# Performance work log

Measured on AMD Instinct MI355X. Metric: run time of the kernel, lower is better.

## Reference

```python
import jax, jax.numpy as jnp
import numpy as np

# Hyper-params from init_kwargs
H, DM, DA, DP, M, T = 8, 512, 256, 128, 32, 4096
DK, DAh, DPh = DM // H, DA // H, DP // H   # 64, 32, 16
B, K_STEPS = 8, 2048
S = T + K_STEPS          # length of x = memory + x_pre
EPS = 1e-12

def _l2n(x):
    # F.normalize(p=2, dim=-1)
    return x / jnp.maximum(jnp.linalg.norm(x, axis=-1, keepdims=True), EPS)

def setup_inputs() -> dict:
    key = jax.random.key(0)
    ks = jax.random.split(key, 28)
    n = lambda i, s, sc=0.05: jax.random.normal(ks[i], s, jnp.float32) * sc
    return {
        "memory": jax.random.normal(ks[0], (B, S - 1, DM), jnp.float32),
        "x_pre":  jax.random.normal(ks[1], (B, 1, DM), jnp.float32),
        "aux":    jax.random.normal(ks[2], (B, S, DA), jnp.float32),
        "pos":    jax.random.normal(ks[3], (B, S, DP), jnp.float32),
        "Wq": n(4, (H, DK, DM)), "bq": n(5, (H, DK)),
        "Wk": n(6, (H, DK, DM)), "bk": n(7, (H, DK)),
        "Wv": n(8, (H, DK, DM)), "bv": n(9, (H, DK)),
        "Wqa": n(10, (H, DAh, DA)), "bqa": n(11, (H, DAh)),
        "Wka": n(12, (H, DAh, DA)), "bka": n(13, (H, DAh)),
        "Wqp": n(14, (H, DPh, DP)), "bqp": n(15, (H, DPh)),
        "Wkp": n(16, (H, DPh, DP)), "bkp": n(17, (H, DPh)),
        "W_ih": n(18, (3 * DK, DM)), "W_hh": n(19, (3 * DK, DK)),
        "b_ih": n(20, (3 * DK,)), "b_hh": n(21, (3 * DK,)),
        "WO": n(22, (DM, DM)), "bO": n(23, (DM,)),
        "w": n(24, (1, 1), 1.0), "w_a": n(25, (1, 1), 1.0), "w_p": n(26, (1, 1), 1.0),
        "G": (jax.random.uniform(ks[27], (DK, DK)) < 0.5).astype(jnp.int32),
        "k": K_STEPS,
    }

def _forward(memory, x_pre, aux, pos, Wq, bq, Wk, bk, Wv, bv, Wqa, bqa, Wka, bka,
             Wqp, bqp, Wkp, bkp, W_ih, W_hh, b_ih, b_hh, WO, bO, w, w_a, w_p, G, k):
    b = memory.shape[0]
    x = jnp.concatenate([memory, x_pre], axis=1)           # [B, S, DM]
    s = x.shape[1]
    Wn = k + T - M + 1                                     # attention window length
    g = G.astype(x.dtype)
    mask_h = jnp.tile(g, (1, H))[None]                     # [1, DK, DM] per-head SparseLinear mask

    # per-head Q/K node projections (SparseLinear), L2-normalized
    Q = _l2n(jnp.einsum('bsd,hkd->bhsk', x, Wq * mask_h) + bq[None, :, None, :])
    K = _l2n(jnp.einsum('bsd,hkd->bhsk', x, Wk * mask_h) + bk[None, :, None, :])

    # tn_transform_pre: for each position p, mean over the M-step window of Qv[m].K[p+m]
    Qv = Q[:, :, -M:, :]                                   # [B,H,M,DK]
    D = jnp.einsum('bhmd,bhsd->bhms', Qv, K)               # [B,H,M,S]
    p_idx = jnp.arange(Wn)[None, :] + jnp.arange(M)[:, None]   # [M,Wn]
    band = D[:, :, jnp.arange(M)[:, None], p_idx]          # [B,H,M,Wn] band-diagonal gather
    tn = band.mean(axis=2)                                 # [B,H,Wn]

    # aux / pos similarities: only the last query row survives the slice in the source
    QA = _l2n(jnp.einsum('bsa,hca->bhsc', aux, Wqa) + bqa[None, :, None, :])
    KA = _l2n(jnp.einsum('bsa,hca->bhsc', aux, Wka) + bka[None, :, None, :])
    dot2 = jnp.einsum('bhc,bhsc->bhs', QA[:, :, -1, :], KA[:, :, aux.shape[1] - Wn:, :])
    QP = _l2n(jnp.einsum('bsp,hcp->bhsc', pos, Wqp) + bqp[None, :, None, :])
    KP = _l2n(jnp.einsum('bsp,hcp->bhsc', pos, Wkp) + bkp[None, :, None, :])
    dot3 = jnp.einsum('bhc,bhsc->bhs', QP[:, :, -1, :], KP[:, :, pos.shape[1] - Wn:, :])

    attn = jax.nn.softmax(w[0, 0] * tn + w_a[0, 0] * dot2 + w_p[0, 0] * dot3, axis=-1)  # [B,H,Wn]

    # value projection over the history window, weighted by attn[..., :-1]
    xv = x[:, s - Wn:s - 1, :]                             # [B, Wn-1, DM]
    V = jnp.einsum('bsd,hkd->bhsk', xv, Wv * mask_h) + bv[None, :, None, :]
    hist = jnp.einsum('bhw,bhwd->bhd', attn[:, :, :-1], V) # [B,H,DK]

    # sequential GRU over the recent M-1 steps (shared across heads)
    recent = jnp.swapaxes(x[:, -M:-1, :], 0, 1)            # [M-1, B, DM]
    def cell(hprev, xt):
        gi = xt @ W_ih.T + b_ih
        gh = hprev @ W_hh.T + b_hh
        ir, iz, inn = jnp.split(gi, 3, axis=-1)
        hr, hz, hn = jnp.split(gh, 3, axis=-1)
        r = jax.nn.sigmoid(ir + hr)
        z = jax.nn.sigmoid(iz + hz)
        nst = jnp.tanh(inn + r * hn)
        return (1.0 - z) * nst + z * hprev, None
    res, _ = jax.lax.scan(cell, jnp.zeros((b, DK), x.dtype), recent)  # [B, DK]

    # concat per-head deltas (deta[:, :, 1:] just drops the initial zeros column)
    deta = (hist + attn[:, :, -1:] * res[:, None, :]).reshape(b, H * DK)   # [B, DM]
    mask_o = jnp.tile(g, (H, H))                           # [DM, DM] for W_O
    out = x_pre + (deta @ (WO * mask_o).T + bO)[:, None, :]
    return out

def reference(memory, x_pre, aux, pos, Wq, bq, Wk, bk, Wv, bv, Wqa, bqa, Wka, bka,
              Wqp, bqp, Wkp, bkp, W_ih, W_hh, b_ih, b_hh, WO, bO, w, w_a, w_p, G, k):
    return _forward(memory, x_pre, aux, pos, Wq, bq, Wk, bk, Wv, bv, Wqa, bqa, Wka,
                    bka, Wqp, bqp, Wkp, bkp, W_ih, W_hh, b_ih, b_hh, WO, bO,
                    w, w_a, w_p, G, k)
```

## Files before the change

kernel.cpp:

```cpp
#include <hip/hip_runtime.h>
#include <math.h>

#define BB   8
#define S    6144
#define SM1  6143
#define DM   512
#define H    8
#define DK   64
#define M    32
#define WN   6113
#define DA   256
#define DAh  32
#define DP   128
#define DPh  16
#define EPSN 1e-12f

#define WS_WKT    0
#define WS_WKAT   262144
#define WS_WKPT   327680
#define WS_QHAT   344064
#define WS_QAHAT  475136
#define WS_QPHAT  477184
#define WS_LOGITS 478208
#define WS_XBAR   869440
#define WS_ALAST  902208
#define WS_RES    902272
#define WS_GI     902784
#define WS_WQM    950400
#define WS_XBF    1212544
#define N_LOGITS  391232
#define N_XBAR    32768

typedef __attribute__((ext_vector_type(8))) short short8;
typedef __attribute__((ext_vector_type(4))) float f32x4;

__device__ inline unsigned short f2bf(float f) {
    union { float f; unsigned u; } v; v.f = f;
    unsigned r = v.u + 0x7fffu + ((v.u >> 16) & 1u);
    return (unsigned short)(r >> 16);
}
__device__ inline float bf2f(unsigned short u) {
    union { unsigned u; float f; } v; v.u = ((unsigned)u) << 16; return v.f;
}

union S8U { short8 v; unsigned short e[8]; };

__global__ void prep_weights(const float* __restrict__ Wk, const float* __restrict__ Wka,
                             const float* __restrict__ Wkp, const float* __restrict__ Wq,
                             const int* __restrict__ G,
                             unsigned short* __restrict__ wkb,
                             unsigned short* __restrict__ wkab,
                             unsigned short* __restrict__ wkpb,
                             float* __restrict__ wqm)
{
    int idx = blockIdx.x * 256 + threadIdx.x;
    if (idx < H*DM*DK) {
        int k = idx & 63; int d = (idx >> 6) & 511; int h = idx >> 15;
        float v = Wk[(size_t)(h*DK + k)*DM + d] * (float)G[k*DK + (d & 63)];
        wkb[(size_t)h*DM*DK + (((d >> 3)*DK + k) << 3) + (d & 7)] = f2bf(v);
    }
    int i2 = idx - H*DM*DK;
    if (i2 >= 0 && i2 < H*DA*DAh) {
        int h = i2 >> 13; int r = i2 & 8191;
        int j = r & 7; int f = r >> 3;
        int c = f & 31; int a = (f >> 5)*8 + j;
        wkab[i2] = f2bf(Wka[(size_t)(h*DAh + c)*DA + a]);
    }
    int i3 = idx - H*DM*DK - H*DA*DAh;
    if (i3 >= 0 && i3 < H*DP*DPh) {
        int h = i3 >> 11; int r = i3 & 2047;
        int j = r & 7; int f = r >> 3;
        int c = f & 15; int p = (f >> 4)*8 + j;
        wkpb[i3] = f2bf(Wkp[(size_t)(h*DPh + c)*DP + p]);
    }
    int i4 = idx - H*DM*DK - H*DA*DAh - H*DP*DPh;
    if (i4 >= 0 && i4 < H*DK*DM) {
        int d = i4 & 511; int k = (i4 >> 9) & 63;
        wqm[i4] = Wq[i4] * (float)G[k*DK + (d & 63)];
    }
}

__global__ __launch_bounds__(256) void xcast_k(
    const float* __restrict__ memory, const float* __restrict__ x_pre,
    unsigned short* __restrict__ xbf)
{
    size_t e = ((size_t)blockIdx.x*256 + threadIdx.x)*8;
    int b = (int)(e / ((size_t)S*DM));
    size_t r = e - (size_t)b*S*DM;
    int t = (int)(r >> 9);
    int d = (int)(r & 511);
    const float* src = (t < SM1) ? memory + ((size_t)b*SM1 + t)*DM + d
                                 : x_pre + (size_t)b*DM + d;
    float4 v0 = *(const float4*)src, v1 = *(const float4*)(src + 4);
    S8U t8;
    t8.e[0]=f2bf(v0.x); t8.e[1]=f2bf(v0.y); t8.e[2]=f2bf(v0.z); t8.e[3]=f2bf(v0.w);
    t8.e[4]=f2bf(v1.x); t8.e[5]=f2bf(v1.y); t8.e[6]=f2bf(v1.z); t8.e[7]=f2bf(v1.w);
    *(short8*)(xbf + e) = t8.v;
}

__global__ __launch_bounds__(256) void qhat_k2(
    const float* __restrict__ memory, const float* __restrict__ x_pre,
    const float* __restrict__ wqm, const float* __restrict__ bq,
    float* __restrict__ qhat)
{
    int bx = blockIdx.x;
    int mp = bx & 15;
    int h  = (bx >> 4) & 7;
    int b  = bx >> 7;
    int tid = threadIdx.x;
    int k = tid & 63, dq = tid >> 6;

    int m0 = mp*2;
    int t0 = S - M + m0, t1 = t0 + 1;
    const float* x0 = ((t0 < SM1) ? memory + ((size_t)b*SM1 + t0)*DM
                                  : x_pre + (size_t)b*DM) + dq*128;
    const float* x1 = ((t1 < SM1) ? memory + ((size_t)b*SM1 + t1)*DM
                                  : x_pre + (size_t)b*DM) + dq*128;
    const float* wr = wqm + (size_t)(h*DK + k)*DM + dq*128;

    float s0 = 0.f, s1 = 0.f;
    #pragma unroll 8
    for (int d = 0; d < 128; d += 4) {
        float4 w4 = *(const float4*)(wr + d);
        float4 a4 = *(const float4*)(x0 + d);
        float4 b4 = *(const float4*)(x1 + d);
        s0 += w4.x*a4.x + w4.y*a4.y + w4.z*a4.z + w4.w*a4.w;
        s1 += w4.x*b4.x + w4.y*b4.y + w4.z*b4.z + w4.w*b4.w;
    }

    __shared__ float part[2][4][64];
    part[0][dq][k] = s0;
    part[1][dq][k] = s1;
    __syncthreads();

    if (tid < 128) {
        int mi = tid >> 6;
        int kk = tid & 63;
        float q = part[mi][0][kk] + part[mi][1][kk] + part[mi][2][kk] + part[mi][3][kk]
                + bq[h*DK + kk];
        float ss = q*q;
        #pragma unroll
        for (int d2 = 1; d2 <= 32; d2 <<= 1) ss += __shfl_xor(ss, d2);
        qhat[((size_t)(b*H + h)*M + (m0 + mi))*DK + kk] = q / fmaxf(sqrtf(ss), EPSN);
    }
}

__global__ __launch_bounds__(256) void qaqp_k(
    const float* __restrict__ aux, const float* __restrict__ pos,
    const float* __restrict__ Wqa, const float* __restrict__ bqa,
    const float* __restrict__ Wqp, const float* __restrict__ bqp,
    float* __restrict__ qahat, float* __restrict__ qphat)
{
    int bh = blockIdx.x; int b = bh >> 3, h = bh & 7;
    int tid = threadIdx.x;
    __shared__ float pa[32][8];
    __shared__ float pp[16][16];

    {
        int c = tid & 31, ch = tid >> 5;
        const float* ar = aux + ((size_t)b*S + (S-1))*DA + ch*32;
        const float* wv = Wqa + (size_t)(h*DAh + c)*DA + ch*32;
        float s = 0.f;
        #pragma unroll
        for (int a = 0; a < 32; a += 4) {
            float4 a4 = *(const float4*)(ar + a);
            float4 w4 = *(const float4*)(wv + a);
            s += a4.x*w4.x + a4.y*w4.y + a4.z*w4.z + a4.w*w4.w;
        }
        pa[c][ch] = s;
    }
    {
        int c = tid & 15, ch = tid >> 4;
        const float* pr = pos + ((size_t)b*S + (S-1))*DP + ch*8;
        const float* wv = Wqp + (size_t)(h*DPh + c)*DP + ch*8;
        float4 a4 = *(const float4*)(pr);
        float4 w4 = *(const float4*)(wv);
        float4 a5 = *(const float4*)(pr + 4);
        float4 w5 = *(const float4*)(wv + 4);
        pp[c][ch] = a4.x*w4.x + a4.y*w4.y + a4.z*w4.z + a4.w*w4.w
                  + a5.x*w5.x + a5.y*w5.y + a5.z*w5.z + a5.w*w5.w;
    }
    __syncthreads();

    if (tid < 32) {
        float q = bqa[h*DAh + tid];
        #pragma unroll
        for (int ch = 0; ch < 8; ++ch) q += pa[tid][ch];
        float ss = q*q;
        #pragma unroll
        for (int d2 = 1; d2 <= 16; d2 <<= 1) ss += __shfl_xor(ss, d2);
        qahat[(size_t)bh*DAh + tid] = q / fmaxf(sqrtf(ss), EPSN);
    } else if (tid >= 64 && tid < 80) {
        int c = tid - 64;
        float q = bqp[h*DPh + c];
        #pragma unroll
        for (int ch = 0; ch < 16; ++ch) q += pp[c][ch];
        float ss = q*q;
        #pragma unroll
        for (int d2 = 1; d2 <= 8; d2 <<= 1) ss += __shfl_xor(ss, d2);
        qphat[(size_t)bh*DPh + c] = q / fmaxf(sqrtf(ss), EPSN);
    }
}

__global__ __launch_bounds__(256, 4) void kproj_mfma3(
    const unsigned short* __restrict__ xbf, const unsigned short* __restrict__ wkb,
    const float* __restrict__ bk, const float* __restrict__ qhat,
    const float* __restrict__ wscal, float* __restrict__ logits)
{
    int bx = blockIdx.x;
    int tile = bx % 96, h = (bx / 96) & 7, b = bx / (96*8);
    int t0 = tile * 64;
    int tid = threadIdx.x;
    int wave = tid >> 6, lane = tid & 63;
    int quad = lane >> 4, l16 = lane & 15;

    __shared__ unsigned short Qs[M][72];
    __shared__ unsigned short Kb[64][72];
    __shared__ float tnloc[95];

    {
        const float* qsrc = qhat + (size_t)(b*H + h)*M*DK;
        int i = tid * 8;
        float4 a0 = *(const float4*)(qsrc + i);
        float4 a1 = *(const float4*)(qsrc + i + 4);
        S8U t8;
        t8.e[0]=f2bf(a0.x); t8.e[1]=f2bf(a0.y); t8.e[2]=f2bf(a0.z); t8.e[3]=f2bf(a0.w);
        t8.e[4]=f2bf(a1.x); t8.e[5]=f2bf(a1.y); t8.e[6]=f2bf(a1.z); t8.e[7]=f2bf(a1.w);
        *(short8*)&Qs[i >> 6][i & 63] = t8.v;
    }
    if (tid < 95) tnloc[tid] = 0.f;

    f32x4 acc[4];
    #pragma unroll
    for (int nt = 0; nt < 4; ++nt) acc[nt] = (f32x4){0.f,0.f,0.f,0.f};

    const unsigned short* xrow = xbf + ((size_t)b*S + t0 + wave*16 + l16)*DM;
    const unsigned short* wh = wkb + (size_t)h*DM*DK;

    #pragma unroll
    for (int ch = 0; ch < 4; ++ch) {
        #pragma unroll
        for (int ks = 0; ks < 4; ++ks) {
            short8 a = *(const short8*)(xrow + ch*128 + ks*32 + quad*8);
            #pragma unroll
            for (int nt = 0; nt < 4; ++nt) {
                short8 bf = *(const short8*)(wh + (((ch*16 + ks*4 + quad)*DK) + nt*16 + l16)*8);
                acc[nt] = __builtin_amdgcn_mfma_f32_16x16x32_bf16(a, bf, acc[nt], 0, 0, 0);
            }
        }
    }

    {
        float vv[4][4];
        float ss[4] = {0.f, 0.f, 0.f, 0.f};
        #pragma unroll
        for (int nt = 0; nt < 4; ++nt) {
            float bkv = bk[h*DK + nt*16 + l16];
            #pragma unroll
            for (int reg = 0; reg < 4; ++reg) {
                float v = acc[nt][reg] + bkv;
                vv[nt][reg] = v;
                ss[reg] += v*v;
            }
        }
        #pragma unroll
        for (int d2 = 1; d2 <= 8; d2 <<= 1)
            #pragma unroll
            for (int reg = 0; reg < 4; ++reg) ss[reg] += __shfl_xor(ss[reg], d2);
        #pragma unroll
        for (int reg = 0; reg < 4; ++reg) {
            float inv = 1.f / fmaxf(sqrtf(ss[reg]), EPSN);
            #pragma unroll
            for (int nt = 0; nt < 4; ++nt)
                Kb[wave*16 + quad*4 + reg][nt*16 + l16] = f2bf(vv[nt][reg] * inv);
        }
    }
    __syncthreads();

    {
        int mtile = wave & 1;
        int thalf = (wave >> 1) * 32;
        f32x4 acc2[2];
        acc2[0] = (f32x4){0.f,0.f,0.f,0.f};
        acc2[1] = (f32x4){0.f,0.f,0.f,0.f};
        #pragma unroll
        for (int ks = 0; ks < 2; ++ks) {
            short8 a = *(const short8*)&Qs[mtile*16 + l16][ks*32 + quad*8];
            #pragma unroll
            for (int nt = 0; nt < 2; ++nt) {
                short8 kf = *(const short8*)&Kb[thalf + nt*16 + l16][ks*32 + quad*8];
                acc2[nt] = __builtin_amdgcn_mfma_f32_16x16x32_bf16(a, kf, acc2[nt], 0, 0, 0);
            }
        }
        int m0 = mtile*16 + quad*4;
        #pragma unroll
        for (int nt = 0; nt < 2; ++nt) {
            int tl = thalf + nt*16 + l16;
            #pragma unroll
            for (int reg = 0; reg < 4; ++reg) {
                int mm = m0 + reg;
                int j = t0 + tl - mm;
                if (j >= 0 && j < WN)
                    atomicAdd(&tnloc[tl - mm + 31], acc2[nt][reg]);
            }
        }
    }
    __syncthreads();
    if (tid < 95) {
        int j = t0 + tid - 31;
        if (j >= 0 && j < WN)
            atomicAdd(&logits[(size_t)(b*H + h)*WN + j], wscal[0]*(1.f/32.f)*tnloc[tid]);
    }
}

__global__ __launch_bounds__(256, 2) void ka_proj_mfma(
    const float* __restrict__ aux, const unsigned short* __restrict__ wkab,
    const float* __restrict__ bka, const float* __restrict__ qahat,
    const float* __restrict__ wa, float* __restrict__ logits)
{
    int tile = blockIdx.x % 96;
    int b    = blockIdx.x / 96;
    int j0   = tile * 64;
    int tid  = threadIdx.x;
    int wave = tid >> 6, lane = tid & 63;
    int quad = lane >> 4, l16 = lane & 15;

    __shared__ unsigned short Xa[32*520];

    {
        int r = tid >> 2, seg = tid & 3;
        int j = j0 + r; if (j > WN-1) j = WN-1;
        const float* ar = aux + ((size_t)b*S + (31 + j))*DA + seg*64;
        int tt = r >> 4, lo = r & 15;
        #pragma unroll
        for (int g = 0; g < 8; ++g) {
            float4 v0 = *(const float4*)(ar + g*8);
            float4 v1 = *(const float4*)(ar + g*8 + 4);
            int d0 = seg*64 + g*8;
            int ks = d0 >> 5, qd = (d0 >> 3) & 3;
            S8U t8;
            t8.e[0]=f2bf(v0.x); t8.e[1]=f2bf(v0.y); t8.e[2]=f2bf(v0.z); t8.e[3]=f2bf(v0.w);
            t8.e[4]=f2bf(v1.x); t8.e[5]=f2bf(v1.y); t8.e[6]=f2bf(v1.z); t8.e[7]=f2bf(v1.w);
            *(short8*)&Xa[(tt*8 + ks)*520 + (qd*16 + lo)*8] = t8.v;
        }
    }
    __syncthreads();

    float wav = wa[0];
    for (int h = 0; h < H; ++h) {
        const unsigned short* wsrc = wkab + (size_t)h*DA*DAh;
        f32x4 acc[2];
        acc[0] = (f32x4){0.f,0.f,0.f,0.f};
        acc[1] = (f32x4){0.f,0.f,0.f,0.f};
        #pragma unroll
        for (int ks = 0; ks < 8; ++ks) {
            short8 a = *(const short8*)&Xa[(wave*8 + ks)*520 + lane*8];
            #pragma unroll
            for (int nt = 0; nt < 2; ++nt) {
                short8 bf = *(const short8*)(wsrc + (size_t)(((ks*4 + quad)*32) + nt*16 + l16)*8);
                acc[nt] = __builtin_amdgcn_mfma_f32_16x16x32_bf16(a, bf, acc[nt], 0, 0, 0);
            }
        }
        float bk0 = bka[h*DAh + l16], bk1 = bka[h*DAh + 16 + l16];
        float q0 = qahat[(size_t)(b*H + h)*DAh + l16];
        float q1 = qahat[(size_t)(b*H + h)*DAh + 16 + l16];
        #pragma unroll
        for (int reg = 0; reg < 4; ++reg) {
            float v0 = acc[0][reg] + bk0;
            float v1 = acc[1][reg] + bk1;
            float ss = v0*v0 + v1*v1;
            float dp = v0*q0 + v1*q1;
            #pragma unroll
            for (int d2 = 1; d2 <= 8; d2 <<= 1) {
                ss += __shfl_xor(ss, d2);
                dp += __shfl_xor(dp, d2);
            }
            if (l16 == 0) {
                int j = j0 + wave*16 + quad*4 + reg;
                if (j < WN)
                    logits[(size_t)(b*H + h)*WN + j] += wav * dp / fmaxf(sqrtf(ss), EPSN);
            }
        }
    }
}

__global__ __launch_bounds__(256, 2) void kp_proj_mfma(
    const float* __restrict__ pos, const unsigned short* __restrict__ wkpb,
    const float* __restrict__ bkp, const float* __restrict__ qphat,
    const float* __restrict__ wp, float* __restrict__ logits)
{
    int tile = blockIdx.x % 96;
    int b    = blockIdx.x / 96;
    int j0   = tile * 64;
    int tid  = threadIdx.x;
    int wave = tid >> 6, lane = tid & 63;
    int quad = lane >> 4, l16 = lane & 15;

    __shared__ unsigned short Xp[16*520];

    {
        int r = tid >> 2, seg = tid & 3;
        int j = j0 + r; if (j > WN-1) j = WN-1;
        const float* pr = pos + ((size_t)b*S + (31 + j))*DP + seg*32;
        int tt = r >> 4, lo = r & 15;
        #pragma unroll
        for (int g = 0; g < 4; ++g) {
            float4 v0 = *(const float4*)(pr + g*8);
            float4 v1 = *(const float4*)(pr + g*8 + 4);
            int d0 = seg*32 + g*8;
            int ks = d0 >> 5, qd = (d0 >> 3) & 3;
            S8U t8;
            t8.e[0]=f2bf(v0.x); t8.e[1]=f2bf(v0.y); t8.e[2]=f2bf(v0.z); t8.e[3]=f2bf(v0.w);
            t8.e[4]=f2bf(v1.x); t8.e[5]=f2bf(v1.y); t8.e[6]=f2bf(v1.z); t8.e[7]=f2bf(v1.w);
            *(short8*)&Xp[(tt*4 + ks)*520 + (qd*16 + lo)*8] = t8.v;
        }
    }
    __syncthreads();

    float wpv = wp[0];
    for (int h = 0; h < H; ++h) {
        const unsigned short* wsrc = wkpb + (size_t)h*DP*DPh;
        f32x4 acc = (f32x4){0.f,0.f,0.f,0.f};
        #pragma unroll
        for (int ks = 0; ks < 4; ++ks) {
            short8 a = *(const short8*)&Xp[(wave*4 + ks)*520 + lane*8];
            short8 bf = *(const short8*)(wsrc + (size_t)(((ks*4 + quad)*16) + l16)*8);
            acc = __builtin_amdgcn_mfma_f32_16x16x32_bf16(a, bf, acc, 0, 0, 0);
        }
        float bk0 = bkp[h*DPh + l16];
        float q0 = qphat[(size_t)(b*H + h)*DPh + l16];
        #pragma unroll
        for (int reg = 0; reg < 4; ++reg) {
            float v = acc[reg] + bk0;
            float ss = v*v;
            float dp = v*q0;
            #pragma unroll
            for (int d2 = 1; d2 <= 8; d2 <<= 1) {
                ss += __shfl_xor(ss, d2);
                dp += __shfl_xor(dp, d2);
            }
            if (l16 == 0) {
                int j = j0 + wave*16 + quad*4 + reg;
                if (j < WN)
                    logits[(size_t)(b*H + h)*WN + j] += wpv * dp / fmaxf(sqrtf(ss), EPSN);
            }
        }
    }
}

__global__ __launch_bounds__(256, 2) void kproj_band_mfma2(
    const float* __restrict__ memory, const float* __restrict__ x_pre,
    const unsigned short* __restrict__ wkb, const float* __restrict__ bk,
    const float* __restrict__ qhat, const float* __restrict__ wscal,
    float* __restrict__ logits)
{
    int bx = blockIdx.x;
    int hp = bx & 3, b = (bx >> 2) & 7, tile = bx >> 5;
    int t0 = tile * 128;
    int tid = threadIdx.x;
    int wave = tid >> 6, lane = tid & 63;
    int quad = lane >> 4, l16 = lane & 15;

    __shared__ unsigned short Xf[32*520];
    __shared__ unsigned short Wf[16*520];
    __shared__ unsigned short Kb[128][72];
    __shared__ unsigned short Qs[M][72];
    __shared__ float tnloc[159];

    if (tid < 159) tnloc[tid] = 0.f;
    {
        int h = hp*2;
        const float* qsrc = qhat + (size_t)(b*H + h)*M*DK;
        int i = tid * 8;
        float4 a0 = *(const float4*)(qsrc + i);
        float4 a1 = *(const float4*)(qsrc + i + 4);
        S8U t8;
        t8.e[0]=f2bf(a0.x); t8.e[1]=f2bf(a0.y); t8.e[2]=f2bf(a0.z); t8.e[3]=f2bf(a0.w);
        t8.e[4]=f2bf(a1.x); t8.e[5]=f2bf(a1.y); t8.e[6]=f2bf(a1.z); t8.e[7]=f2bf(a1.w);
        *(short8*)&Qs[i >> 6][i & 63] = t8.v;
    }

    f32x4 acc[2][2][4];
    #pragma unroll
    for (int hi = 0; hi < 2; ++hi)
        #pragma unroll
        for (int mt = 0; mt < 2; ++mt)
            #pragma unroll
            for (int nt = 0; nt < 4; ++nt) acc[hi][mt][nt] = (f32x4){0.f,0.f,0.f,0.f};

    for (int ch = 0; ch < 4; ++ch) {
        __syncthreads();
        {
            int r = tid >> 1, half = tid & 1;
            int t = t0 + r;
            const float* xr = ((t < SM1) ? (memory + ((size_t)b*SM1 + t)*DM)
                                         : (x_pre + (size_t)b*DM)) + ch*128 + half*64;
            int tt = r >> 4, lo = r & 15;
            #pragma unroll
            for (int g = 0; g < 8; ++g) {
                float4 v0 = *(const float4*)(xr + g*8);
                float4 v1 = *(const float4*)(xr + g*8 + 4);
                int d0 = half*64 + g*8;
                int ks = d0 >> 5, qd = (d0 >> 3) & 3;
                S8U t8;
                t8.e[0]=f2bf(v0.x); t8.e[1]=f2bf(v0.y); t8.e[2]=f2bf(v0.z); t8.e[3]=f2bf(v0.w);
                t8.e[4]=f2bf(v1.x); t8.e[5]=f2bf(v1.y); t8.e[6]=f2bf(v1.z); t8.e[7]=f2bf(v1.w);
                *(short8*)&Xf[(tt*4 + ks)*520 + (qd*16 + lo)*8] = t8.v;
            }
        }
        {
            const unsigned short* src = wkb + (size_t)(hp*2)*DM*DK + (size_t)ch*8192;
            #pragma unroll
            for (int i = 0; i < 4; ++i) {
                int f = tid + 256*i;
                *(short8*)&Wf[(f >> 6)*520 + (f & 63)*8] = *(const short8*)(src + f*8);
            }
        }
        __syncthreads();
        #pragma unroll
        for (int ks = 0; ks < 4; ++ks) {
            short8 a0 = *(const short8*)&Xf[((wave*2 + 0)*4 + ks)*520 + lane*8];
            short8 a1 = *(const short8*)&Xf[((wave*2 + 1)*4 + ks)*520 + lane*8];
            #pragma unroll
            for (int nt = 0; nt < 4; ++nt) {
                short8 bf = *(const short8*)&Wf[(ks*4 + quad)*520 + (nt*16 + l16)*8];
                acc[0][0][nt] = __builtin_amdgcn_mfma_f32_16x16x32_bf16(a0, bf, acc[0][0][nt], 0, 0, 0);
                acc[0][1][nt] = __builtin_amdgcn_mfma_f32_16x16x32_bf16(a1, bf, acc[0][1][nt], 0, 0, 0);
            }
        }
        __syncthreads();
        {
            const unsigned short* src = wkb + (size_t)(hp*2 + 1)*DM*DK + (size_t)ch*8192;
            #pragma unroll
            for (int i = 0; i < 4; ++i) {
                int f = tid + 256*i;
                *(short8*)&Wf[(f >> 6)*520 + (f & 63)*8] = *(const short8*)(src + f*8);
            }
        }
        __syncthreads();
        #pragma unroll
        for (int ks = 0; ks < 4; ++ks) {
            short8 a0 = *(const short8*)&Xf[((wave*2 + 0)*4 + ks)*520 + lane*8];
            short8 a1 = *(const short8*)&Xf[((wave*2 + 1)*4 + ks)*520 + lane*8];
            #pragma unroll
            for (int nt = 0; nt < 4; ++nt) {
                short8 bf = *(const short8*)&Wf[(ks*4 + quad)*520 + (nt*16 + l16)*8];
                acc[1][0][nt] = __builtin_amdgcn_mfma_f32_16x16x32_bf16(a0, bf, acc[1][0][nt], 0, 0, 0);
                acc[1][1][nt] = __builtin_amdgcn_mfma_f32_16x16x32_bf16(a1, bf, acc[1][1][nt], 0, 0, 0);
            }
        }
    }

    float wom = wscal[0] * (1.f/32.f);

    for (int hi = 0; hi < 2; ++hi) {
        int h = hp*2 + hi;
        __syncthreads();
        {
            float ss[2][4];
            float vv[2][4][4];
            #pragma unroll
            for (int mt = 0; mt < 2; ++mt)
                #pragma unroll
                for (int reg = 0; reg < 4; ++reg) ss[mt][reg] = 0.f;
            #pragma unroll
            for (int nt = 0; nt < 4; ++nt) {
                float bkv = bk[h*DK + nt*16 + l16];
                #pragma unroll
                for (int mt = 0; mt < 2; ++mt)
                    #pragma unroll
                    for (int reg = 0; reg < 4; ++reg) {
                        float v = acc[hi][mt][nt][reg] + bkv;
                        vv[mt][nt][reg] = v;
                        ss[mt][reg] += v*v;
                    }
            }
            #pragma unroll
            for (int d2 = 1; d2 <= 8; d2 <<= 1)
                #pragma unroll
                for (int mt = 0; mt < 2; ++mt)
                    #pragma unroll
                    for (int reg = 0; reg < 4; ++reg)
                        ss[mt][reg] += __shfl_xor(ss[mt][reg], d2);
            #pragma unroll
            for (int mt = 0; mt < 2; ++mt) {
                float inv[4];
                #pragma unroll
                for (int reg = 0; reg < 4; ++reg)
                    inv[reg] = 1.f / fmaxf(sqrtf(ss[mt][reg]), EPSN);
                #pragma unroll
                for (int nt = 0; nt < 4; ++nt)
                    #pragma unroll
                    for (int reg = 0; reg < 4; ++reg)
                        Kb[wave*32 + mt*16 + quad*4 + reg][nt*16 + l16] =
                            f2bf(vv[mt][nt][reg] * inv[reg]);
            }
        }
        __syncthreads();
        {
            f32x4 acc2[2][2];
            #pragma unroll
            for (int mt = 0; mt < 2; ++mt)
                #pragma unroll
                for (int nt = 0; nt < 2; ++nt) acc2[mt][nt] = (f32x4){0.f,0.f,0.f,0.f};
            #pragma unroll
            for (int ks = 0; ks < 2; ++ks) {
                short8 qa0 = *(const short8*)&Qs[l16     ][ks*32 + quad*8];
                short8 qa1 = *(const short8*)&Qs[16 + l16][ks*32 + quad*8];
                #pragma unroll
                for (int nt = 0; nt < 2; ++nt) {
                    short8 kf = *(const short8*)&Kb[wave*32 + nt*16 + l16][ks*32 + quad*8];
                    acc2[0][nt] = __builtin_amdgcn_mfma_f32_16x16x32_bf16(qa0, kf, acc2[0][nt], 0, 0, 0);
                    acc2[1][nt] = __builtin_amdgcn_mfma_f32_16x16x32_bf16(qa1, kf, acc2[1][nt], 0, 0, 0);
                }
            }
            #pragma unroll
            for (int mt = 0; mt < 2; ++mt)
                #pragma unroll
                for (int nt = 0; nt < 2; ++nt) {
                    int tcol = wave*32 + nt*16 + l16;
                    #pragma unroll
                    for (int reg = 0; reg < 4; ++reg) {
                        int m = mt*16 + quad*4 + reg;
                        int j = t0 + tcol - m;
                        if (j >= 0 && j < WN)
                            atomicAdd(&tnloc[tcol - m + 31], acc2[mt][nt][reg]);
                    }
                }
        }
        __syncthreads();
        if (tid < 159) {
            int j = t0 + tid - 31;
            if (j >= 0 && j < WN)
                atomicAdd(&logits[(size_t)(b*H + h)*WN + j], wom * tnloc[tid]);
            tnloc[tid] = 0.f;
        }
        if (hi == 0) {
            const float* qsrc = qhat + (size_t)(b*H + h + 1)*M*DK;
            int i = tid * 8;
            float4 a0 = *(const float4*)(qsrc + i);
            float4 a1 = *(const float4*)(qsrc + i + 4);
            S8U t8;
            t8.e[0]=f2bf(a0.x); t8.e[1]=f2bf(a0.y); t8.e[2]=f2bf(a0.z); t8.e[3]=f2bf(a0.w);
            t8.e[4]=f2bf(a1.x); t8.e[5]=f2bf(a1.y); t8.e[6]=f2bf(a1.z); t8.e[7]=f2bf(a1.w);
            *(short8*)&Qs[i >> 6][i & 63] = t8.v;
        }
    }
}

__global__ __launch_bounds__(256) void softmax_k(float* __restrict__ logits,
                                                 float* __restrict__ alast)
{
    int bh = blockIdx.x;
    float* L = logits + (size_t)bh*WN;
    __shared__ float red[256];
    int tid = threadIdx.x;
    float mx = -1e30f;
    for (int j = tid; j < WN; j += 256) mx = fmaxf(mx, L[j]);
    red[tid] = mx; __syncthreads();
    for (int s2 = 128; s2 > 0; s2 >>= 1) {
        if (tid < s2) red[tid] = fmaxf(red[tid], red[tid+s2]);
        __syncthreads();
    }
    mx = red[0]; __syncthreads();
    float sm = 0.f;
    for (int j = tid; j < WN; j += 256) sm += expf(L[j] - mx);
    red[tid] = sm; __syncthreads();
    for (int s2 = 128; s2 > 0; s2 >>= 1) {
        if (tid < s2) red[tid] += red[tid+s2];
        __syncthreads();
    }
    float inv = 1.f / red[0];
    for (int j = tid; j < WN; j += 256) {
        float a = expf(L[j] - mx) * inv;
        L[j] = a;
        if (j == WN-1) alast[bh] = a;
    }
}

#define JC 191
__global__ __launch_bounds__(256) void xbar_bf_k(
    const unsigned short* __restrict__ xbf, const float* __restrict__ attn,
    float* __restrict__ xbar)
{
    int chunk = blockIdx.x & 31;
    int b = blockIdx.x >> 5;
    int j0 = chunk * JC;
    __shared__ float al[H][JC];
    int tid = threadIdx.x;
    for (int i = tid; i < H*JC; i += 256) {
        int hh = i / JC, jj = i - hh*JC;
        al[hh][jj] = attn[(size_t)(b*H + hh)*WN + j0 + jj];
    }
    __syncthreads();
    int d0 = tid * 2;
    const unsigned* p = (const unsigned*)(xbf + ((size_t)b*S + 31 + j0)*DM + d0);
    float acc[H][2];
    #pragma unroll
    for (int hh = 0; hh < H; ++hh) { acc[hh][0] = 0.f; acc[hh][1] = 0.f; }
    for (int jj = 0; jj < JC; ++jj) {
        unsigned u = p[(size_t)jj*(DM/2)];
        float x0 = bf2f((unsigned short)(u & 0xffff));
        float x1 = bf2f((unsigned short)(u >> 16));
        #pragma unroll
        for (int hh = 0; hh < H; ++hh) {
            float a = al[hh][jj];
            acc[hh][0] += a * x0;
            acc[hh][1] += a * x1;
        }
    }
    #pragma unroll
    for (int hh = 0; hh < H; ++hh) {
        atomicAdd(&xbar[(size_t)(b*H+hh)*DM + d0],     acc[hh][0]);
        atomicAdd(&xbar[(size_t)(b*H+hh)*DM + d0 + 1], acc[hh][1]);
    }
}

__global__ __launch_bounds__(256) void xbar_k(
    const float* __restrict__ memory, const float* __restrict__ attn,
    float* __restrict__ xbar)
{
    int chunk = blockIdx.x & 31;
    int b = blockIdx.x >> 5;
    int j0 = chunk * JC;
    __shared__ float al[H][JC];
    int tid = threadIdx.x;
    for (int i = tid; i < H*JC; i += 256) {
        int hh = i / JC, jj = i - hh*JC;
        al[hh][jj] = attn[(size_t)(b*H + hh)*WN + j0 + jj];
    }
    __syncthreads();
    int d0 = tid * 2;
    float acc[H][2];
    #pragma unroll
    for (int hh = 0; hh < H; ++hh) { acc[hh][0] = 0.f; acc[hh][1] = 0.f; }
    for (int jj = 0; jj < JC; ++jj) {
        int t = 31 + j0 + jj;
        const float2 xv = *(const float2*)(memory + ((size_t)b*SM1 + t)*DM + d0);
        #pragma unroll
        for (int hh = 0; hh < H; ++hh) {
            float a = al[hh][jj];
            acc[hh][0] += a * xv.x;
            acc[hh][1] += a * xv.y;
        }
    }
    #pragma unroll
    for (int hh = 0; hh < H; ++hh) {
        atomicAdd(&xbar[(size_t)(b*H+hh)*DM + d0],     acc[hh][0]);
        atomicAdd(&xbar[(size_t)(b*H+hh)*DM + d0 + 1], acc[hh][1]);
    }
}

__global__ __launch_bounds__(192) void gi_k(
    const float* __restrict__ memory, const float* __restrict__ W_ih,
    const float* __restrict__ b_ih, float* __restrict__ gi_all)
{
    int t = blockIdx.x >> 3;
    int b = blockIdx.x & 7;
    int c = threadIdx.x;
    const float* xr = memory + ((size_t)b*SM1 + (S - M) + t)*DM;
    const float* wr = W_ih + (size_t)c*DM;
    float s = b_ih[c];
    for (int d = 0; d < DM; d += 4) {
        float4 x4 = *(const float4*)(xr + d);
        float4 w4 = *(const float4*)(wr + d);
        s += x4.x*w4.x + x4.y*w4.y + x4.z*w4.z + x4.w*w4.w;
    }
    gi_all[((size_t)t*BB + b)*192 + c] = s;
}

__global__ __launch_bounds__(512) void gru_scan(
    const float* __restrict__ gi_all, const float* __restrict__ W_hh,
    const float* __restrict__ b_hh, float* __restrict__ res)
{
    int b = threadIdx.x >> 6;
    int l = threadIdx.x & 63;

    float w0[64], w1[64], w2[64];
    {
        const float* r0p = W_hh + (size_t)l*DK;
        const float* r1p = W_hh + (size_t)(64 + l)*DK;
        const float* r2p = W_hh + (size_t)(128 + l)*DK;
        #pragma unroll
        for (int i = 0; i < 16; ++i) {
            float4 a = *(const float4*)(r0p + i*4);
            w0[i*4]=a.x; w0[i*4+1]=a.y; w0[i*4+2]=a.z; w0[i*4+3]=a.w;
            float4 c = *(const float4*)(r1p + i*4);
            w1[i*4]=c.x; w1[i*4+1]=c.y; w1[i*4+2]=c.z; w1[i*4+3]=c.w;
            float4 e = *(const float4*)(r2p + i*4);
            w2[i*4]=e.x; w2[i*4+1]=e.y; w2[i*4+2]=e.z; w2[i*4+3]=e.w;
        }
    }
    float bh0 = b_hh[l], bh1 = b_hh[64 + l], bh2 = b_hh[128 + l];

    float h = 0.f;
    const float* g0 = gi_all + (size_t)b*192;
    float gr = g0[l], gz = g0[64 + l], gn = g0[128 + l];

    #pragma unroll 1
    for (int t = 0; t < 31; ++t) {
        float a0 = bh0, a1 = bh1, a2 = bh2;
        #pragma unroll
        for (int k = 0; k < 64; ++k) {
            float hk = __int_as_float(__builtin_amdgcn_readlane(__float_as_int(h), k));
            a0 += hk * w0[k];
            a1 += hk * w1[k];
            a2 += hk * w2[k];
        }
        float ngr = 0.f, ngz = 0.f, ngn = 0.f;
        if (t < 30) {
            const float* g2 = gi_all + ((size_t)(t+1)*BB + b)*192;
            ngr = g2[l]; ngz = g2[64 + l]; ngn = g2[128 + l];
        }
        float r = 1.f / (1.f + expf(-(gr + a0)));
        float z = 1.f / (1.f + expf(-(gz + a1)));
        float n = tanhf(gn + r * a2);
        h = (1.f - z)*n + z*h;
        gr = ngr; gz = ngz; gn = ngn;
    }
    res[b*DK + l] = h;
}

__global__ __launch_bounds__(512) void final_k(
    const float* __restrict__ x_pre, const float* __restrict__ xbar,
    const float* __restrict__ Wv, const float* __restrict__ bv,
    const float* __restrict__ WO, const float* __restrict__ bO,
    const float* __restrict__ alast, const float* __restrict__ res,
    const int* __restrict__ G, float* __restrict__ out)
{
    int b = blockIdx.x;
    int tid = threadIdx.x;
    __shared__ float gl[64*64];
    __shared__ float deta[512];
    for (int i = tid; i < 4096; i += 512) gl[i] = (float)G[(i & 63)*64 + (i >> 6)];
    __syncthreads();
    int h = tid >> 6, dk = tid & 63;
    float ala = alast[b*H + h];
    const float* xb  = xbar + (size_t)(b*H + h)*DM;
    const float* wvr = Wv + (size_t)tid*DM;
    const float* gcol = gl + dk;
    float s = 0.f;
    for (int e = 0; e < DM; e += 4) {
        float4 wv4 = *(const float4*)(wvr + e);
        float4 xb4 = *(const float4*)(xb + e);
        int eb = e & 63;
        s += wv4.x*gcol[eb*64]     *xb4.x + wv4.y*gcol[(eb+1)*64]*xb4.y
           + wv4.z*gcol[(eb+2)*64]*xb4.z + wv4.w*gcol[(eb+3)*64]*xb4.w;
    }
    float hist = s + bv[tid]*(1.f - ala);
    deta[tid] = hist + ala * res[b*DK + dk];
    __syncthreads();
    int dpos = tid;
    const float* wor = WO + (size_t)dpos*DM;
    const float* gcol2 = gl + (dpos & 63);
    float o = 0.f;
    for (int jj = 0; jj < DM; jj += 4) {
        float4 wo4 = *(const float4*)(wor + jj);
        int jb = jj & 63;
        o += wo4.x*gcol2[jb*64]     *deta[jj]   + wo4.y*gcol2[(jb+1)*64]*deta[jj+1]
           + wo4.z*gcol2[(jb+2)*64]*deta[jj+2] + wo4.w*gcol2[(jb+3)*64]*deta[jj+3];
    }
    out[(size_t)b*DM + dpos] = x_pre[(size_t)b*DM + dpos] + o + bO[dpos];
}

extern "C" void kernel_launch(void* const* d_in, const int* in_sizes, int n_in,
                              void* d_out, int out_size, void* d_ws, size_t ws_size,
                              hipStream_t stream)
{
    const float* memory = (const float*)d_in[0];
    const float* x_pre  = (const float*)d_in[1];
    const float* aux    = (const float*)d_in[2];
    const float* pos    = (const float*)d_in[3];
    const float* Wq  = (const float*)d_in[4];
    const float* bq  = (const float*)d_in[5];
    const float* Wk  = (const float*)d_in[6];
    const float* bk  = (const float*)d_in[7];
    const float* Wv  = (const float*)d_in[8];
    const float* bv  = (const float*)d_in[9];
    const float* Wqa = (const float*)d_in[10];
    const float* bqa = (const float*)d_in[11];
    const float* Wka = (const float*)d_in[12];
    const float* bka = (const float*)d_in[13];
    const float* Wqp = (const float*)d_in[14];
    const float* bqp = (const float*)d_in[15];
    const float* Wkp = (const float*)d_in[16];
    const float* bkp = (const float*)d_in[17];
    const float* W_ih = (const float*)d_in[18];
    const float* W_hh = (const float*)d_in[19];
    const float* b_ih = (const float*)d_in[20];
    const float* b_hh = (const float*)d_in[21];
    const float* WO  = (const float*)d_in[22];
    const float* bO  = (const float*)d_in[23];
    const float* w   = (const float*)d_in[24];
    const float* w_a = (const float*)d_in[25];
    const float* w_p = (const float*)d_in[26];
    const int*   G   = (const int*)d_in[27];
    (void)in_sizes; (void)n_in; (void)out_size;

    float* ws = (float*)d_ws;
    unsigned short* wkb  = (unsigned short*)(ws + WS_WKT);
    unsigned short* wkab = (unsigned short*)(ws + WS_WKAT);
    unsigned short* wkpb = (unsigned short*)(ws + WS_WKPT);
    float* qhat   = ws + WS_QHAT;
    float* qahat  = ws + WS_QAHAT;
    float* qphat  = ws + WS_QPHAT;
    float* logits = ws + WS_LOGITS;
    float* xbar   = ws + WS_XBAR;
    float* alast  = ws + WS_ALAST;
    float* resb   = ws + WS_RES;
    float* gi_all = ws + WS_GI;
    float* wqm    = ws + WS_WQM;
    unsigned short* xbf = (unsigned short*)(ws + WS_XBF);
    float* outp   = (float*)d_out;

    const size_t need = ((size_t)WS_XBF + 12582912) * 4;
    const bool big = (ws_size >= need);

    hipMemsetAsync(logits, 0, (size_t)(N_LOGITS + N_XBAR)*sizeof(float), stream);

    prep_weights<<<(H*DM*DK + H*DA*DAh + H*DP*DPh + H*DK*DM + 255)/256, 256, 0, stream>>>(
        Wk, Wka, Wkp, Wq, G, wkb, wkab, wkpb, wqm);

    if (big)
        xcast_k<<<12288, 256, 0, stream>>>(memory, x_pre, xbf);

    gi_k<<<31*BB, 192, 0, stream>>>(memory, W_ih, b_ih, gi_all);
    gru_scan<<<1, 512, 0, stream>>>(gi_all, W_hh, b_hh, resb);

    qhat_k2<<<BB*H*16, 256, 0, stream>>>(memory, x_pre, wqm, bq, qhat);
    qaqp_k<<<BB*H, 256, 0, stream>>>(aux, pos, Wqa, bqa, Wqp, bqp, qahat, qphat);

    if (big)
        kproj_mfma3<<<96*8*BB, 256, 0, stream>>>(xbf, wkb, bk, qhat, w, logits);
    else
        kproj_band_mfma2<<<48*BB*4, 256, 0, stream>>>(memory, x_pre, wkb, bk, qhat,
                                                      w, logits);

    ka_proj_mfma<<<BB*96, 256, 0, stream>>>(aux, wkab, bka, qahat, w_a, logits);
    kp_proj_mfma<<<BB*96, 256, 0, stream>>>(pos, wkpb, bkp, qphat, w_p, logits);

    softmax_k<<<BB*H, 256, 0, stream>>>(logits, alast);

    if (big)
        xbar_bf_k<<<BB*32, 256, 0, stream>>>(xbf, logits, xbar);
    else
        xbar_k<<<BB*32, 256, 0, stream>>>(memory, logits, xbar);

    final_k<<<BB, 512, 0, stream>>>(x_pre, xbar, Wv, bv, WO, bO, alast, resb, G, outp);
}
```

Before: 614.0 us.

## Retile K projection so one block covers all heads with shared A tiles

The bf16 copy of x is rewritten into a k-slot-major layout of 8-element groups, produced through a shared-memory transpose. The K projection kernel now runs 512-thread blocks where each wave handles one head for a 64-row tile. Activation tiles are loaded once into double-buffered LDS and reused across all eight heads, instead of each head's block re-reading x. Q is pre-packed into bf16 MFMA fragment order by a new qhat kernel, and the Kb tile uses XOR swizzling against bank conflicts. This adds per-step barriers, a larger register footprint (16 accumulators per wave), and a layout change that the xbar kernel must also follow.

```diff
diff --git a/kernel.cpp b/kernel.cpp
--- a/kernel.cpp
+++ b/kernel.cpp
@@ -80,22 +80,44 @@
     }
 }
 
-__global__ __launch_bounds__(256) void xcast_k(
+__global__ __launch_bounds__(256) void xcast2_k(
     const float* __restrict__ memory, const float* __restrict__ x_pre,
-    unsigned short* __restrict__ xbf)
-{
-    size_t e = ((size_t)blockIdx.x*256 + threadIdx.x)*8;
-    int b = (int)(e / ((size_t)S*DM));
-    size_t r = e - (size_t)b*S*DM;
-    int t = (int)(r >> 9);
-    int d = (int)(r & 511);
-    const float* src = (t < SM1) ? memory + ((size_t)b*SM1 + t)*DM + d
-                                 : x_pre + (size_t)b*DM + d;
-    float4 v0 = *(const float4*)src, v1 = *(const float4*)(src + 4);
-    S8U t8;
-    t8.e[0]=f2bf(v0.x); t8.e[1]=f2bf(v0.y); t8.e[2]=f2bf(v0.z); t8.e[3]=f2bf(v0.w);
-    t8.e[4]=f2bf(v1.x); t8.e[5]=f2bf(v1.y); t8.e[6]=f2bf(v1.z); t8.e[7]=f2bf(v1.w);
-    *(short8*)(xbf + e) = t8.v;
+    unsigned short* __restrict__ xbf2)
+{
+    int tile = blockIdx.x % 96;
+    int b    = blockIdx.x / 96;
+    int t0 = tile * 64;
+    int tid = threadIdx.x;
+    __shared__ __align__(16) unsigned short T[64][72];
+
+    int tr = tid >> 2, seg = tid & 3;
+    int t  = t0 + tr;
+    const float* src = (t < SM1) ? memory + ((size_t)b*SM1 + t)*DM
+                                 : x_pre + (size_t)b*DM;
+
+    for (int dch = 0; dch < 8; ++dch) {
+        const float* p = src + dch*64 + seg*16;
+        float4 v0 = *(const float4*)(p);
+        float4 v1 = *(const float4*)(p + 4);
+        float4 v2 = *(const float4*)(p + 8);
+        float4 v3 = *(const float4*)(p + 12);
+        S8U a, c;
+        a.e[0]=f2bf(v0.x); a.e[1]=f2bf(v0.y); a.e[2]=f2bf(v0.z); a.e[3]=f2bf(v0.w);
+        a.e[4]=f2bf(v1.x); a.e[5]=f2bf(v1.y); a.e[6]=f2bf(v1.z); a.e[7]=f2bf(v1.w);
+        c.e[0]=f2bf(v2.x); c.e[1]=f2bf(v2.y); c.e[2]=f2bf(v2.z); c.e[3]=f2bf(v2.w);
+        c.e[4]=f2bf(v3.x); c.e[5]=f2bf(v3.y); c.e[6]=f2bf(v3.z); c.e[7]=f2bf(v3.w);
+        *(short8*)&T[tr][seg*16]     = a.v;
+        *(short8*)&T[tr][seg*16 + 8] = c.v;
+        __syncthreads();
+        #pragma unroll
+        for (int it = 0; it < 2; ++it) {
+            int cidx = tid + it*256;
+            int slot = cidx >> 6, tw = cidx & 63;
+            short8 v = *(const short8*)&T[tw][slot*8];
+            *(short8*)(xbf2 + ((size_t)(b*64 + dch*8 + slot)*S + t0 + tw)*8) = v;
+        }
+        __syncthreads();
+    }
 }
 
 __global__ __launch_bounds__(256) void qhat_k2(
@@ -142,6 +164,55 @@
         #pragma unroll
         for (int d2 = 1; d2 <= 32; d2 <<= 1) ss += __shfl_xor(ss, d2);
         qhat[((size_t)(b*H + h)*M + (m0 + mi))*DK + kk] = q / fmaxf(sqrtf(ss), EPSN);
+    }
+}
+
+__global__ __launch_bounds__(256) void qhat_k2b(
+    const float* __restrict__ memory, const float* __restrict__ x_pre,
+    const float* __restrict__ wqm, const float* __restrict__ bq,
+    unsigned short* __restrict__ qbf)
+{
+    int bx = blockIdx.x;
+    int mp = bx & 15;
+    int h  = (bx >> 4) & 7;
+    int b  = bx >> 7;
+    int tid = threadIdx.x;
+    int k = tid & 63, dq = tid >> 6;
+
+    int m0 = mp*2;
+    int t0 = S - M + m0, t1 = t0 + 1;
+    const float* x0 = ((t0 < SM1) ? memory + ((size_t)b*SM1 + t0)*DM
+                                  : x_pre + (size_t)b*DM) + dq*128;
+    const float* x1 = ((t1 < SM1) ? memory + ((size_t)b*SM1 + t1)*DM
+                                  : x_pre + (size_t)b*DM) + dq*128;
+    const float* wr = wqm + (size_t)(h*DK + k)*DM + dq*128;
+
+    float s0 = 0.f, s1 = 0.f;
+    #pragma unroll 8
+    for (int d = 0; d < 128; d += 4) {
+        float4 w4 = *(const float4*)(wr + d);
+        float4 a4 = *(const float4*)(x0 + d);
+        float4 b4 = *(const float4*)(x1 + d);
+        s0 += w4.x*a4.x + w4.y*a4.y + w4.z*a4.z + w4.w*a4.w;
+        s1 += w4.x*b4.x + w4.y*b4.y + w4.z*b4.z + w4.w*b4.w;
+    }
+
+    __shared__ float part[2][4][64];
+    part[0][dq][k] = s0;
+    part[1][dq][k] = s1;
+    __syncthreads();
+
+    if (tid < 128) {
+        int mi = tid >> 6;
+        int kk = tid & 63;
+        float q = part[mi][0][kk] + part[mi][1][kk] + part[mi][2][kk] + part[mi][3][kk]
+                + bq[h*DK + kk];
+        float ss = q*q;
+        #pragma unroll
+        for (int d2 = 1; d2 <= 32; d2 <<= 1) ss += __shfl_xor(ss, d2);
+        float qn = q / fmaxf(sqrtf(ss), EPSN);
+        int ks = kk >> 5, qd = (kk >> 3) & 3, j = kk & 7;
+        qbf[((size_t)(((b*H + h)*2 + ks)*4 + qd)*32 + (m0 + mi))*8 + j] = f2bf(qn);
     }
 }
 
@@ -202,114 +273,144 @@
     }
 }
 
-__global__ __launch_bounds__(256, 4) void kproj_mfma3(
-    const unsigned short* __restrict__ xbf, const unsigned short* __restrict__ wkb,
-    const float* __restrict__ bk, const float* __restrict__ qhat,
+__global__ __launch_bounds__(512, 4) void kproj_mfma5(
+    const unsigned short* __restrict__ xbf2, const unsigned short* __restrict__ wkb,
+    const float* __restrict__ bk, const unsigned short* __restrict__ qbf,
     const float* __restrict__ wscal, float* __restrict__ logits)
 {
-    int bx = blockIdx.x;
-    int tile = bx % 96, h = (bx / 96) & 7, b = bx / (96*8);
+    int tile = blockIdx.x % 96;
+    int b    = blockIdx.x / 96;
     int t0 = tile * 64;
     int tid = threadIdx.x;
     int wave = tid >> 6, lane = tid & 63;
     int quad = lane >> 4, l16 = lane & 15;
-
-    __shared__ unsigned short Qs[M][72];
-    __shared__ unsigned short Kb[64][72];
-    __shared__ float tnloc[95];
-
-    {
-        const float* qsrc = qhat + (size_t)(b*H + h)*M*DK;
-        int i = tid * 8;
-        float4 a0 = *(const float4*)(qsrc + i);
-        float4 a1 = *(const float4*)(qsrc + i + 4);
-        S8U t8;
-        t8.e[0]=f2bf(a0.x); t8.e[1]=f2bf(a0.y); t8.e[2]=f2bf(a0.z); t8.e[3]=f2bf(a0.w);
-        t8.e[4]=f2bf(a1.x); t8.e[5]=f2bf(a1.y); t8.e[6]=f2bf(a1.z); t8.e[7]=f2bf(a1.w);
-        *(short8*)&Qs[i >> 6][i & 63] = t8.v;
-    }
-    if (tid < 95) tnloc[tid] = 0.f;
-
-    f32x4 acc[4];
+    int h = wave;
+
+    __shared__ __align__(16) unsigned short As[2][8][64][8];
+    __shared__ __align__(16) unsigned short Kb[H][32][64];
+    __shared__ float tnloc[H][95];
+
+    for (int i = tid; i < H*95; i += 512) ((float*)tnloc)[i] = 0.f;
+
+    const unsigned short* asrc = xbf2 + ((size_t)(b*64 + wave)*S + t0 + lane)*8;
+    short8 sreg = *(const short8*)asrc;
+    *(short8*)&As[0][wave][lane][0] = sreg;
+    __syncthreads();
+
+    f32x4 acc[4][4];
     #pragma unroll
-    for (int nt = 0; nt < 4; ++nt) acc[nt] = (f32x4){0.f,0.f,0.f,0.f};
-
-    const unsigned short* xrow = xbf + ((size_t)b*S + t0 + wave*16 + l16)*DM;
+    for (int mt = 0; mt < 4; ++mt)
+        #pragma unroll
+        for (int nt = 0; nt < 4; ++nt) acc[mt][nt] = (f32x4){0.f,0.f,0.f,0.f};
+
     const unsigned short* wh = wkb + (size_t)h*DM*DK;
 
+    #pragma unroll 2
+    for (int kc = 0; kc < 8; ++kc) {
+        int buf = kc & 1;
+        if (kc < 7) sreg = *(const short8*)(asrc + (size_t)(kc+1)*8*S*8);
+        #pragma unroll
+        for (int ks = 0; ks < 2; ++ks) {
+            int kslot = ks*4 + quad;
+            short8 bfrag[4];
+            #pragma unroll
+            for (int nt = 0; nt < 4; ++nt)
+                bfrag[nt] = *(const short8*)(wh +
+                    (size_t)(((kc*2 + ks)*4 + quad)*DK + nt*16 + l16)*8);
+            short8 afrag[4];
+            #pragma unroll
+            for (int mt = 0; mt < 4; ++mt)
+                afrag[mt] = *(const short8*)&As[buf][kslot][mt*16 + l16][0];
+            #pragma unroll
+            for (int mt = 0; mt < 4; ++mt)
+                #pragma unroll
+                for (int nt = 0; nt < 4; ++nt)
+                    acc[mt][nt] = __builtin_amdgcn_mfma_f32_16x16x32_bf16(
+                        afrag[mt], bfrag[nt], acc[mt][nt], 0, 0, 0);
+        }
+        __syncthreads();
+        if (kc < 7) {
+            *(short8*)&As[buf^1][wave][lane][0] = sreg;
+            __syncthreads();
+        }
+    }
+
+    float bkc[4];
     #pragma unroll
-    for (int ch = 0; ch < 4; ++ch) {
-        #pragma unroll
-        for (int ks = 0; ks < 4; ++ks) {
-            short8 a = *(const short8*)(xrow + ch*128 + ks*32 + quad*8);
-            #pragma unroll
-            for (int nt = 0; nt < 4; ++nt) {
-                short8 bf = *(const short8*)(wh + (((ch*16 + ks*4 + quad)*DK) + nt*16 + l16)*8);
-                acc[nt] = __builtin_amdgcn_mfma_f32_16x16x32_bf16(a, bf, acc[nt], 0, 0, 0);
-            }
-        }
-    }
-
-    {
-        float vv[4][4];
-        float ss[4] = {0.f, 0.f, 0.f, 0.f};
-        #pragma unroll
-        for (int nt = 0; nt < 4; ++nt) {
-            float bkv = bk[h*DK + nt*16 + l16];
+    for (int nt = 0; nt < 4; ++nt) bkc[nt] = bk[h*DK + nt*16 + l16];
+    float wom = wscal[0] * (1.f/32.f);
+
+    #pragma unroll
+    for (int half = 0; half < 2; ++half) {
+        __syncthreads();
+        #pragma unroll
+        for (int mh = 0; mh < 2; ++mh) {
+            int mt = half*2 + mh;
+            float ss[4] = {0.f,0.f,0.f,0.f};
+            #pragma unroll
+            for (int nt = 0; nt < 4; ++nt)
+                #pragma unroll
+                for (int reg = 0; reg < 4; ++reg) {
+                    float v = acc[mt][nt][reg] + bkc[nt];
+                    ss[reg] += v*v;
+                }
+            #pragma unroll
+            for (int d2 = 1; d2 <= 8; d2 <<= 1)
+                #pragma unroll
+                for (int reg = 0; reg < 4; ++reg) ss[reg] += __shfl_xor(ss[reg], d2);
             #pragma unroll
             for (int reg = 0; reg < 4; ++reg) {
-                float v = acc[nt][reg] + bkv;
-                vv[nt][reg] = v;
-                ss[reg] += v*v;
-            }
-        }
-        #pragma unroll
-        for (int d2 = 1; d2 <= 8; d2 <<= 1)
-            #pragma unroll
-            for (int reg = 0; reg < 4; ++reg) ss[reg] += __shfl_xor(ss[reg], d2);
-        #pragma unroll
-        for (int reg = 0; reg < 4; ++reg) {
-            float inv = 1.f / fmaxf(sqrtf(ss[reg]), EPSN);
-            #pragma unroll
-            for (int nt = 0; nt < 4; ++nt)
-                Kb[wave*16 + quad*4 + reg][nt*16 + l16] = f2bf(vv[nt][reg] * inv);
-        }
+                float inv = 1.f / fmaxf(sqrtf(ss[reg]), EPSN);
+                int rih = mh*16 + quad*4 + reg;
+                #pragma unroll
+                for (int nt = 0; nt < 4; ++nt) {
+                    int col = nt*16 + l16;
+                    int colsw = (((col >> 3) ^ (rih & 7)) << 3) | (col & 7);
+                    Kb[h][rih][colsw] = f2bf((acc[mt][nt][reg] + bkc[nt]) * inv);
+                }
+            }
+        }
+        __syncthreads();
+        f32x4 a2[2][2];
+        #pragma unroll
+        for (int mt2 = 0; mt2 < 2; ++mt2)
+            #pragma unroll
+            for (int nt2 = 0; nt2 < 2; ++nt2) a2[mt2][nt2] = (f32x4){0.f,0.f,0.f,0.f};
+        #pragma unroll
+        for (int ks2 = 0; ks2 < 2; ++ks2) {
+            short8 kf[2];
+            #pragma unroll
+            for (int nt2 = 0; nt2 < 2; ++nt2) {
+                int rih = nt2*16 + l16;
+                int slot = (ks2*4 + quad) ^ (rih & 7);
+                kf[nt2] = *(const short8*)&Kb[h][rih][slot*8];
+            }
+            #pragma unroll
+            for (int mt2 = 0; mt2 < 2; ++mt2) {
+                short8 qa = *(const short8*)(qbf +
+                    (size_t)((((b*H + h)*2 + ks2)*4 + quad)*32 + mt2*16 + l16)*8);
+                a2[mt2][0] = __builtin_amdgcn_mfma_f32_16x16x32_bf16(qa, kf[0], a2[mt2][0], 0, 0, 0);
+                a2[mt2][1] = __builtin_amdgcn_mfma_f32_16x16x32_bf16(qa, kf[1], a2[mt2][1], 0, 0, 0);
+            }
+        }
+        #pragma unroll
+        for (int mt2 = 0; mt2 < 2; ++mt2)
+            #pragma unroll
+            for (int nt2 = 0; nt2 < 2; ++nt2) {
+                int tl = half*32 + nt2*16 + l16;
+                #pragma unroll
+                for (int reg = 0; reg < 4; ++reg) {
+                    int m = mt2*16 + quad*4 + reg;
+                    atomicAdd(&tnloc[h][tl - m + 31], a2[mt2][nt2][reg]);
+                }
+            }
     }
     __syncthreads();
-
-    {
-        int mtile = wave & 1;
-        int thalf = (wave >> 1) * 32;
-        f32x4 acc2[2];
-        acc2[0] = (f32x4){0.f,0.f,0.f,0.f};
-        acc2[1] = (f32x4){0.f,0.f,0.f,0.f};
-        #pragma unroll
-        for (int ks = 0; ks < 2; ++ks) {
-            short8 a = *(const short8*)&Qs[mtile*16 + l16][ks*32 + quad*8];
-            #pragma unroll
-            for (int nt = 0; nt < 2; ++nt) {
-                short8 kf = *(const short8*)&Kb[thalf + nt*16 + l16][ks*32 + quad*8];
-                acc2[nt] = __builtin_amdgcn_mfma_f32_16x16x32_bf16(a, kf, acc2[nt], 0, 0, 0);
-            }
-        }
-        int m0 = mtile*16 + quad*4;
-        #pragma unroll
-        for (int nt = 0; nt < 2; ++nt) {
-            int tl = thalf + nt*16 + l16;
-            #pragma unroll
-            for (int reg = 0; reg < 4; ++reg) {
-                int mm = m0 + reg;
-                int j = t0 + tl - mm;
-                if (j >= 0 && j < WN)
-                    atomicAdd(&tnloc[tl - mm + 31], acc2[nt][reg]);
-            }
-        }
-    }
-    __syncthreads();
-    if (tid < 95) {
-        int j = t0 + tid - 31;
+    for (int i = tid; i < H*95; i += 512) {
+        int hh = i / 95, dd = i - hh*95;
+        int j = t0 + dd - 31;
         if (j >= 0 && j < WN)
-            atomicAdd(&logits[(size_t)(b*H + h)*WN + j], wscal[0]*(1.f/32.f)*tnloc[tid]);
+            atomicAdd(&logits[(size_t)(b*H + hh)*WN + j], wom * tnloc[hh][dd]);
     }
 }
 
@@ -679,8 +780,8 @@
 }
 
 #define JC 191
-__global__ __launch_bounds__(256) void xbar_bf_k(
-    const unsigned short* __restrict__ xbf, const float* __restrict__ attn,
+__global__ __launch_bounds__(256) void xbar_bf_k2(
+    const unsigned short* __restrict__ xbf2, const float* __restrict__ attn,
     float* __restrict__ xbar)
 {
     int chunk = blockIdx.x & 31;
@@ -694,12 +795,14 @@
     }
     __syncthreads();
     int d0 = tid * 2;
-    const unsigned* p = (const unsigned*)(xbf + ((size_t)b*S + 31 + j0)*DM + d0);
+    int dslot = d0 >> 3;
+    const unsigned* p = (const unsigned*)(xbf2 +
+        ((size_t)(b*64 + dslot)*S + 31 + j0)*8 + (d0 & 7));
     float acc[H][2];
     #pragma unroll
     for (int hh = 0; hh < H; ++hh) { acc[hh][0] = 0.f; acc[hh][1] = 0.f; }
     for (int jj = 0; jj < JC; ++jj) {
-        unsigned u = p[(size_t)jj*(DM/2)];
+        unsigned u = p[jj*4];
         float x0 = bf2f((unsigned short)(u & 0xffff));
         float x1 = bf2f((unsigned short)(u >> 16));
         #pragma unroll
@@ -902,6 +1005,7 @@
     unsigned short* wkab = (unsigned short*)(ws + WS_WKAT);
     unsigned short* wkpb = (unsigned short*)(ws + WS_WKPT);
     float* qhat   = ws + WS_QHAT;
+    unsigned short* qbf = (unsigned short*)(ws + WS_QHAT);
     float* qahat  = ws + WS_QAHAT;
     float* qphat  = ws + WS_QPHAT;
     float* logits = ws + WS_LOGITS;
@@ -910,7 +1014,7 @@
     float* resb   = ws + WS_RES;
     float* gi_all = ws + WS_GI;
     float* wqm    = ws + WS_WQM;
-    unsigned short* xbf = (unsigned short*)(ws + WS_XBF);
+    unsigned short* xbf2 = (unsigned short*)(ws + WS_XBF);
     float* outp   = (float*)d_out;
 
     const size_t need = ((size_t)WS_XBF + 12582912) * 4;
@@ -922,16 +1026,19 @@
         Wk, Wka, Wkp, Wq, G, wkb, wkab, wkpb, wqm);
 
     if (big)
-        xcast_k<<<12288, 256, 0, stream>>>(memory, x_pre, xbf);
+        xcast2_k<<<BB*96, 256, 0, stream>>>(memory, x_pre, xbf2);
 
     gi_k<<<31*BB, 192, 0, stream>>>(memory, W_ih, b_ih, gi_all);
     gru_scan<<<1, 512, 0, stream>>>(gi_all, W_hh, b_hh, resb);
 
-    qhat_k2<<<BB*H*16, 256, 0, stream>>>(memory, x_pre, wqm, bq, qhat);
+    if (big)
+        qhat_k2b<<<BB*H*16, 256, 0, stream>>>(memory, x_pre, wqm, bq, qbf);
+    else
+        qhat_k2<<<BB*H*16, 256, 0, stream>>>(memory, x_pre, wqm, bq, qhat);
     qaqp_k<<<BB*H, 256, 0, stream>>>(aux, pos, Wqa, bqa, Wqp, bqp, qahat, qphat);
 
     if (big)
-        kproj_mfma3<<<96*8*BB, 256, 0, stream>>>(xbf, wkb, bk, qhat, w, logits);
+        kproj_mfma5<<<BB*96, 512, 0, stream>>>(xbf2, wkb, bk, qbf, w, logits);
     else
         kproj_band_mfma2<<<48*BB*4, 256, 0, stream>>>(memory, x_pre, wkb, bk, qhat,
                                                       w, logits);
@@ -942,7 +1049,7 @@
     softmax_k<<<BB*H, 256, 0, stream>>>(logits, alast);
 
     if (big)
-        xbar_bf_k<<<BB*32, 256, 0, stream>>>(xbf, logits, xbar);
+        xbar_bf_k2<<<BB*32, 256, 0, stream>>>(xbf2, logits, xbar);
     else
         xbar_k<<<BB*32, 256, 0, stream>>>(memory, logits, xbar);
 
```

New measurement: 634.9 us. 3.4% more time.
